# Kernel optimization log

Measured on AMD Instinct MI355X. Metric: run time of the kernel, lower is better.

Reference implementation:

```python
import jax, jax.numpy as jnp
import numpy as np
from jax import lax

GN_EPS = 1e-5
LRELU_SLOPE = 0.2
TOP_K = 3
COMMITMENT = 0.25
NUM_CODES = 1024

def conv(x, w, b, stride=1, pad=1):
    y = lax.conv_general_dilated(x, w, (stride, stride), ((pad, pad), (pad, pad)),
                                 dimension_numbers=('NCHW', 'OIHW', 'NCHW'))
    return y + b[None, :, None, None]

def conv_transpose(x, w, b, stride=2, pad=1, out_pad=1):
    # torch ConvTranspose2d: w is (Cin, Cout, kH, kW); equivalent to lhs-dilated conv
    # with flipped, io-swapped kernel and padding k-1-p (plus out_pad on high side).
    k = w.shape[2]
    p = k - 1 - pad
    w_f = jnp.transpose(jnp.flip(w, (2, 3)), (1, 0, 2, 3))  # -> OIHW
    y = lax.conv_general_dilated(x, w_f, (1, 1), ((p, p + out_pad), (p, p + out_pad)),
                                 lhs_dilation=(stride, stride),
                                 dimension_numbers=('NCHW', 'OIHW', 'NCHW'))
    return y + b[None, :, None, None]

def group_norm(x, g, beta, groups=2):
    N, C, H, W = x.shape
    xg = x.reshape(N, groups, C // groups, H, W)
    mu = xg.mean((2, 3, 4), keepdims=True)
    var = xg.var((2, 3, 4), keepdims=True)
    xn = ((xg - mu) * lax.rsqrt(var + GN_EPS)).reshape(N, C, H, W)
    return xn * g[None, :, None, None] + beta[None, :, None, None]

def lrelu(x):
    return jnp.where(x >= 0, x, LRELU_SLOPE * x)

def vq_ema_eval(z, emb):
    # z: [B, D, H, W] -> tokens [N, D]; eval path (no EMA buffer updates)
    inputs = jnp.transpose(z, (0, 2, 3, 1))  # [B,H,W,D]
    flat = inputs.reshape(-1, emb.shape[1])
    d = (jnp.sum(flat ** 2, 1, keepdims=True) + jnp.sum(emb ** 2, 1)
         - 2.0 * flat @ emb.T)  # [N, K]
    _, idx = lax.top_k(-d, TOP_K)  # top_k smallest distances
    q0 = emb[idx[:, 0]].reshape(inputs.shape)
    e_latent_loss = jnp.mean((lax.stop_gradient(q0) - inputs) ** 2)
    loss = COMMITMENT * e_latent_loss
    quantized = inputs + lax.stop_gradient(q0 - inputs)  # straight-through
    # perplexity uses the LAST (k-th nearest) encodings, matching the torch loop
    last = idx[:, TOP_K - 1]
    counts = jnp.zeros((emb.shape[0],), flat.dtype).at[last].add(1.0)
    avg_probs = counts / flat.shape[0]
    perplexity = jnp.exp(-jnp.sum(avg_probs * jnp.log(avg_probs + 1e-10)))
    return loss, jnp.transpose(quantized, (0, 3, 1, 2)), perplexity

def setup_inputs() -> dict:
    key = jax.random.key(0)
    ks = jax.random.split(key, 16)
    s = 0.05
    d = {
        'x': jax.random.normal(ks[0], (4, 4, 96, 96), jnp.float32),
        'e0_w': jax.random.normal(ks[1], (128, 4, 3, 3), jnp.float32) * s,
        'e0_b': jnp.zeros((128,), jnp.float32),
        'e0_g': jnp.ones((128,), jnp.float32),
        'e0_beta': jnp.zeros((128,), jnp.float32),
        'e1_w': jax.random.normal(ks[2], (128, 128, 3, 3), jnp.float32) * s,
        'e1_b': jnp.zeros((128,), jnp.float32),
        'e1_g': jnp.ones((128,), jnp.float32),
        'e1_beta': jnp.zeros((128,), jnp.float32),
        'pv_w': jax.random.normal(ks[3], (128, 128, 1, 1), jnp.float32) * s,
        'pv_b': jnp.zeros((128,), jnp.float32),
        'emb': jax.random.normal(ks[4], (NUM_CODES, 128), jnp.float32),
        'd0_w': jax.random.normal(ks[5], (128, 128, 3, 3), jnp.float32) * s,  # ConvT: (Cin,Cout,k,k)
        'd0_b': jnp.zeros((128,), jnp.float32),
        'd0_g': jnp.ones((128,), jnp.float32),
        'd0_beta': jnp.zeros((128,), jnp.float32),
        'd1_w': jax.random.normal(ks[6], (128, 256, 3, 3), jnp.float32) * s,
        'd1_b': jnp.zeros((128,), jnp.float32),
        'd1_g': jnp.ones((128,), jnp.float32),
        'd1_beta': jnp.zeros((128,), jnp.float32),
        'proj_w': jax.random.normal(ks[7], (128, 128, 1, 1), jnp.float32) * s,
        'proj_b': jnp.zeros((128,), jnp.float32),
        'ro_w': jax.random.normal(ks[8], (4, 128, 1, 1), jnp.float32) * s,
        'ro_b': jnp.zeros((4,), jnp.float32),
    }
    return d

def reference(x, e0_w, e0_b, e0_g, e0_beta, e1_w, e1_b, e1_g, e1_beta,
              pv_w, pv_b, emb,
              d0_w, d0_b, d0_g, d0_beta, d1_w, d1_b, d1_g, d1_beta,
              proj_w, proj_b, ro_w, ro_b):
    # Encoder: strides [1, 2]
    enc1 = lrelu(group_norm(conv(x, e0_w, e0_b, stride=1, pad=1), e0_g, e0_beta))
    latent = lrelu(group_norm(conv(enc1, e1_w, e1_b, stride=2, pad=1), e1_g, e1_beta))
    z = conv(latent, pv_w, pv_b, stride=1, pad=0)
    loss, quantized, perplexity = vq_ema_eval(z, emb)
    # Decoder: strides [2, 1]; skip projected (embedding_dim != C_out)
    skip = conv(enc1, proj_w, proj_b, stride=1, pad=0)
    h = lrelu(group_norm(conv_transpose(quantized, d0_w, d0_b, stride=2, pad=1, out_pad=1), d0_g, d0_beta))
    y = lrelu(group_norm(conv(jnp.concatenate([h, skip], axis=1), d1_w, d1_b, stride=1, pad=1), d1_g, d1_beta))
    x_recon = conv(y, ro_w, ro_b, stride=1, pad=0)
    return (loss, x_recon, perplexity)
```

## Files before the change

### kernel.cpp

```cpp
#include <hip/hip_runtime.h>

#define DEVI __device__ __forceinline__

typedef unsigned short u16;
typedef __attribute__((ext_vector_type(8))) short bf8v;
typedef __attribute__((ext_vector_type(4))) short s4v;
typedef __attribute__((ext_vector_type(4))) float f4v;

constexpr int NB = 4, C = 128, H = 96, W = 96, HW = H * W;
constexpr int HL = 48, WL = 48, HWL = HL * WL;
constexpr int CODES = 1024, DIM = 128;
constexpr int ROWS = NB * HWL;

DEVI float lrelu_f(float v) { return v >= 0.f ? v : 0.2f * v; }

DEVI u16 f2bf(float f) {
  union { float f; unsigned u; } v; v.f = f;
  unsigned r = (v.u + 0x7FFFu + ((v.u >> 16) & 1u)) >> 16;
  return (u16)r;
}

DEVI float bf2f(u16 h) {
  union { unsigned u; float f; } v; v.u = (unsigned)h << 16;
  return v.f;
}

DEVI void wave_red2(float& s, float& s2) {
#pragma unroll
  for (int o = 32; o > 0; o >>= 1) { s += __shfl_down(s, o); s2 += __shfl_down(s2, o); }
}

DEVI bool block_red2(float& s, float& s2) {
  wave_red2(s, s2);
  __shared__ float ls[8], ls2[8];
  int wv = threadIdx.x >> 6, ln = threadIdx.x & 63;
  if (ln == 0) { ls[wv] = s; ls2[wv] = s2; }
  __syncthreads();
  if (threadIdx.x == 0) {
    s = ls[0] + ls[1] + ls[2] + ls[3];
    s2 = ls2[0] + ls2[1] + ls2[2] + ls2[3];
    return true;
  }
  return false;
}

DEVI void ins3(float e, int j, float& d0, int& i0, float& d1, int& i1, float& d2, int& i2) {
  bool b0 = (e < d0) || (e == d0 && j < i0);
  bool b1 = (e < d1) || (e == d1 && j < i1);
  bool b2 = (e < d2) || (e == d2 && j < i2);
  float nd0 = b0 ? e : d0;             int ni0 = b0 ? j : i0;
  float nd1 = b0 ? d0 : (b1 ? e : d1); int ni1 = b0 ? i0 : (b1 ? j : i1);
  float nd2 = b1 ? d1 : (b2 ? e : d2); int ni2 = b1 ? i1 : (b2 ? j : i2);
  d0 = nd0; i0 = ni0; d1 = nd1; i1 = ni1; d2 = nd2; i2 = ni2;
}

__global__ __launch_bounds__(256) void k_red16(const float2* __restrict__ src,
                                               float* __restrict__ dst, int per) {
  int slot = blockIdx.x;
  float s = 0.f, s2 = 0.f;
  for (int i = threadIdx.x; i < per; i += 256) {
    float2 v = src[(size_t)slot * per + i];
    s += v.x; s2 += v.y;
  }
  if (block_red2(s, s2)) { dst[slot * 2] = s; dst[slot * 2 + 1] = s2; }
}

__global__ __launch_bounds__(256) void k_pack_all(
    const float* __restrict__ d1_w, const float* __restrict__ d0_w,
    const float* __restrict__ pj_w, const float* __restrict__ emb,
    const float* __restrict__ e1_w,
    u16* __restrict__ A1, u16* __restrict__ A0, u16* __restrict__ Apj,
    u16* __restrict__ ehtil, u16* __restrict__ We1,
    float* __restrict__ enorm, float* __restrict__ counts) {
  int b = blockIdx.x, t = threadIdx.x;
  if (b < 1152) {
    int i = b * 256 + t;
    int ci = i & 31, co = (i >> 5) & 127, r = i >> 12;
    int kx = r % 3; int r2 = r / 3; int ch = r2 & 7, ky = r2 >> 3;
    A1[i] = f2bf(d1_w[((size_t)(co * 256 + ch * 32 + ci) * 3 + ky) * 3 + kx]);
  } else if (b < 1728) {
    int i = (b - 1152) * 256 + t;
    int ci = i & 31, co = (i >> 5) & 127, r = i >> 12;
    int wx = r % 3; int r2 = r / 3; int ch = r2 & 3, wy = r2 >> 2;
    A0[i] = f2bf(d0_w[((size_t)((ch * 32 + ci) * 128 + co) * 3 + wy) * 3 + wx]);
  } else if (b < 1792) {
    int i = (b - 1728) * 256 + t;
    int ci = i & 31, co = (i >> 5) & 127, ch = i >> 12;
    Apj[i] = f2bf(pj_w[co * 128 + ch * 32 + ci]);
  } else if (b < 1920) {
    int g = (b - 1792) * 256 + t;
    int ct = g >> 9; int rem = g & 511;
    int j = rem >> 6; int l = rem & 63;
    int code = ct * 16 + (l & 15);
    int kb = j * 32 + (l >> 4) * 8;
    bool lo = kb >= 128; int k0 = lo ? kb - 128 : kb;
    const float* ep = emb + (size_t)code * DIM + k0;
    u16 o[8];
#pragma unroll
    for (int e = 0; e < 8; ++e) {
      float v = ep[e];
      u16 h = f2bf(v);
      o[e] = lo ? f2bf(v - bf2f(h)) : h;
    }
    bf8v ov = {(short)o[0], (short)o[1], (short)o[2], (short)o[3],
               (short)o[4], (short)o[5], (short)o[6], (short)o[7]};
    *(bf8v*)&ehtil[(size_t)g * 8] = ov;
  } else if (b < 1924) {
    int e = (b - 1920) * 256 + t;
    const float4* p = (const float4*)(emb + (size_t)e * DIM);
    float s = 0.f;
#pragma unroll 8
    for (int i = 0; i < 32; ++i) {
      float4 v = p[i];
      s = fmaf(v.x, v.x, s); s = fmaf(v.y, v.y, s); s = fmaf(v.z, v.z, s); s = fmaf(v.w, v.w, s);
    }
    enorm[e] = s;
  } else if (b == 1924) {
#pragma unroll
    for (int k = 0; k < 4; ++k) counts[t + k * 256] = 0.f;
  } else {
    int p = (b - 1925) * 256 + t;
    int s = p >> 6, l = p & 63;
    int ct = s & 7; int r = s >> 3;
    int kx = r % 3; int r2 = r / 3; int ch = r2 & 3, ky = r2 >> 2;
    int co = ct * 16 + (l & 15), ci0 = ch * 32 + (l >> 4) * 8;
    u16 hh[8], ll[8];
#pragma unroll
    for (int e = 0; e < 8; ++e) {
      float v = e1_w[((size_t)(co * 128 + ci0 + e) * 3 + ky) * 3 + kx];
      u16 h = f2bf(v); hh[e] = h; ll[e] = f2bf(v - bf2f(h));
    }
    bf8v hv = {(short)hh[0], (short)hh[1], (short)hh[2], (short)hh[3],
               (short)hh[4], (short)hh[5], (short)hh[6], (short)hh[7]};
    bf8v lv = {(short)ll[0], (short)ll[1], (short)ll[2], (short)ll[3],
               (short)ll[4], (short)ll[5], (short)ll[6], (short)ll[7]};
    *(bf8v*)&We1[(size_t)s * 1024 + l * 8] = hv;
    *(bf8v*)&We1[(size_t)s * 1024 + 512 + l * 8] = lv;
  }
}

__global__ __launch_bounds__(256) void k_conv_e0t(
    const float* __restrict__ x, const float* __restrict__ wg,
    const float* __restrict__ bias, float* __restrict__ out, float2* __restrict__ ps) {
  __shared__ float xs[4][18][104];
  int b = blockIdx.x;
  int rq = b % 6; int co = (b / 6) & 127; int n = b / 768;
  int t = threadIdx.x;
  int tx = t & 15, r = t >> 4;
  int y0 = rq * 16;
  for (int e = t; e < 4 * 18 * 104; e += 256) {
    int ci = e / 1872; int rem = e - ci * 1872;
    int row = rem / 104; int off = rem - row * 104;
    int iy = y0 - 1 + row; int ix = off - 1;
    float v = 0.f;
    if ((unsigned)iy < 96u && (unsigned)ix < 96u)
      v = x[((size_t)(n * 4 + ci)) * HW + iy * 96 + ix];
    xs[ci][row][off] = v;
  }
  float wr[4][9];
  const float* wp = wg + co * 36;
#pragma unroll
  for (int ci = 0; ci < 4; ++ci)
#pragma unroll
    for (int k = 0; k < 9; ++k) wr[ci][k] = wp[ci * 9 + k];
  float bv = bias[co];
  __syncthreads();
  float acc[6];
#pragma unroll
  for (int p = 0; p < 6; ++p) acc[p] = bv;
#pragma unroll
  for (int ci = 0; ci < 4; ++ci) {
#pragma unroll
    for (int ky = 0; ky < 3; ++ky) {
      const float* rp = &xs[ci][r + ky][6 * tx];
      float f[8];
#pragma unroll
      for (int j = 0; j < 4; ++j) {
        float2 v2 = *(const float2*)(rp + 2 * j);
        f[2 * j] = v2.x; f[2 * j + 1] = v2.y;
      }
      float w0 = wr[ci][ky * 3 + 0], w1 = wr[ci][ky * 3 + 1], w2 = wr[ci][ky * 3 + 2];
#pragma unroll
      for (int p = 0; p < 6; ++p)
        acc[p] = fmaf(w0, f[p], fmaf(w1, f[p + 1], fmaf(w2, f[p + 2], acc[p])));
    }
  }
  float* op = out + ((size_t)(n * 128 + co) * 96 + (y0 + r)) * 96 + 6 * tx;
#pragma unroll
  for (int j = 0; j < 3; ++j) {
    float2 v2 = { acc[2 * j], acc[2 * j + 1] };
    *(float2*)(op + 2 * j) = v2;
  }
  float s = 0.f, s2 = 0.f;
#pragma unroll
  for (int p = 0; p < 6; ++p) { s += acc[p]; s2 += acc[p] * acc[p]; }
  if (block_red2(s, s2)) {
    int slot = n * 2 + (co >> 6);
    ps[(size_t)slot * 384 + (co & 63) * 6 + rq] = make_float2(s, s2);
  }
}

__global__ __launch_bounds__(256) void k_gn_px(
    const float* __restrict__ enc1, const float* __restrict__ stats,
    const float* __restrict__ gam, const float* __restrict__ bet, u16* __restrict__ xp) {
  int b = blockIdx.x;
  int ch = b & 3; int iy = (b >> 2) % 96; int n = b / 384;
  int t = threadIdx.x;
  const float invc = 1.f / (64.f * 9216.f);
  size_t chunk = ((size_t)((n * 96 + iy) * 4 + ch)) * 6208;
  for (int e = t; e < 388; e += 256) {
    int oct = e / 97, u = e - oct * 97;
    int ix = (u < 48) ? 2 * u : 2 * (u - 48) - 1;
    u16* dh = xp + chunk + u * 32 + oct * 8;
    u16* dl = dh + 3104;
    if (ix < 0) {
      bf8v z = {0, 0, 0, 0, 0, 0, 0, 0};
      *(bf8v*)dh = z; *(bf8v*)dl = z;
      continue;
    }
    u16 hh[8], ll[8];
#pragma unroll
    for (int e8 = 0; e8 < 8; ++e8) {
      int c = ch * 32 + oct * 8 + e8;
      const float* st = stats + (n * 2 + (c >> 6)) * 2;
      float mu = st[0] * invc;
      float var = fmaf(-mu, mu, st[1] * invc);
      float rs = rsqrtf(var + 1e-5f);
      float raw = enc1[((size_t)(n * 128 + c)) * 9216 + iy * 96 + ix];
      float v = lrelu_f(fmaf((raw - mu) * rs, gam[c], bet[c]));
      u16 h = f2bf(v); hh[e8] = h; ll[e8] = f2bf(v - bf2f(h));
    }
    bf8v hv = {(short)hh[0], (short)hh[1], (short)hh[2], (short)hh[3],
               (short)hh[4], (short)hh[5], (short)hh[6], (short)hh[7]};
    bf8v lv = {(short)ll[0], (short)ll[1], (short)ll[2], (short)ll[3],
               (short)ll[4], (short)ll[5], (short)ll[6], (short)ll[7]};
    *(bf8v*)dh = hv; *(bf8v*)dl = lv;
  }
}

__global__ __launch_bounds__(256) void k_conv_e1m(
    const u16* __restrict__ xp, const u16* __restrict__ We1,
    const float* __restrict__ bias, float* __restrict__ latent, float2* __restrict__ ps) {
  __shared__ float ls[4], ls2[4];
  int braw = blockIdx.x;
  int b = (braw & 7) * 48 + (braw >> 3);
  int cb = b & 1; int oy = (b >> 1) % 48; int n = b / 96;
  int t = threadIdx.x; int w = t >> 6; int lane = t & 63;
  int ln16 = lane & 15, quad = lane >> 4;
  int ctg = cb * 4 + w;
  f4v acc[3];
#pragma unroll
  for (int nt = 0; nt < 3; ++nt) acc[nt] = (f4v){0.f, 0.f, 0.f, 0.f};
  for (int ky = 0; ky < 3; ++ky) {
    int iy = 2 * oy + ky - 1;
    if ((unsigned)iy >= 96u) continue;
    for (int ch = 0; ch < 4; ++ch) {
      const u16* chunk = xp + ((size_t)((n * 96 + iy) * 4 + ch)) * 6208;
      const u16* wb = We1 + ((size_t)((ky * 4 + ch) * 3)) * 8192;
      bf8v ah[3], al[3];
#pragma unroll
      for (int kx = 0; kx < 3; ++kx) {
        const u16* sl = wb + (kx * 8 + ctg) * 1024 + lane * 8;
        ah[kx] = *(const bf8v*)sl;
        al[kx] = *(const bf8v*)(sl + 512);
      }
#pragma unroll
      for (int nt = 0; nt < 3; ++nt) {
        int px = nt * 16 + ln16;
        const u16* be = chunk + px * 32 + quad * 8;
        const u16* bo = chunk + (48 + px) * 32 + quad * 8;
        bf8v bhe  = *(const bf8v*)be;
        bf8v ble  = *(const bf8v*)(be + 3104);
        bf8v bho0 = *(const bf8v*)bo;
        bf8v blo0 = *(const bf8v*)(bo + 3104);
        bf8v bho1 = *(const bf8v*)(bo + 32);
        bf8v blo1 = *(const bf8v*)(bo + 32 + 3104);
        acc[nt] = __builtin_amdgcn_mfma_f32_16x16x32_bf16(ah[1], bhe, acc[nt], 0, 0, 0);
        acc[nt] = __builtin_amdgcn_mfma_f32_16x16x32_bf16(al[1], bhe, acc[nt], 0, 0, 0);
        acc[nt] = __builtin_amdgcn_mfma_f32_16x16x32_bf16(ah[1], ble, acc[nt], 0, 0, 0);
        acc[nt] = __builtin_amdgcn_mfma_f32_16x16x32_bf16(ah[0], bho0, acc[nt], 0, 0, 0);
        acc[nt] = __builtin_amdgcn_mfma_f32_16x16x32_bf16(al[0], bho0, acc[nt], 0, 0, 0);
        acc[nt] = __builtin_amdgcn_mfma_f32_16x16x32_bf16(ah[0], blo0, acc[nt], 0, 0, 0);
        acc[nt] = __builtin_amdgcn_mfma_f32_16x16x32_bf16(ah[2], bho1, acc[nt], 0, 0, 0);
        acc[nt] = __builtin_amdgcn_mfma_f32_16x16x32_bf16(al[2], bho1, acc[nt], 0, 0, 0);
        acc[nt] = __builtin_amdgcn_mfma_f32_16x16x32_bf16(ah[2], blo1, acc[nt], 0, 0, 0);
      }
    }
  }
  int co0 = cb * 64 + w * 16 + quad * 4;
  float4 bv = *(const float4*)&bias[co0];
  float s = 0.f, s2 = 0.f;
#pragma unroll
  for (int nt = 0; nt < 3; ++nt) {
    int px = nt * 16 + ln16;
#pragma unroll
    for (int g = 0; g < 4; ++g) {
      float bvg = (g == 0) ? bv.x : (g == 1) ? bv.y : (g == 2) ? bv.z : bv.w;
      float v = acc[nt][g] + bvg;
      latent[((size_t)(n * 128 + co0 + g)) * 2304 + oy * 48 + px] = v;
      s += v; s2 += v * v;
    }
  }
  wave_red2(s, s2);
  if (lane == 0) { ls[w] = s; ls2[w] = s2; }
  __syncthreads();
  if (t == 0) {
    int slot = n * 2 + cb;
    ps[(size_t)slot * 48 + oy] =
        make_float2(ls[0] + ls[1] + ls[2] + ls[3], ls2[0] + ls2[1] + ls2[2] + ls2[3]);
  }
}

__global__ __launch_bounds__(256) void k_gn_nhwc_bf(
    const float* __restrict__ in, u16* __restrict__ outb, const float* __restrict__ stats,
    const float* __restrict__ gam, const float* __restrict__ bet) {
  int idx = blockIdx.x * 256 + threadIdx.x;
  int c = idx & 127;
  int n = idx / (9216 * 128);
  const float* st = stats + (n * 2 + (c >> 6)) * 2;
  const float invcnt = 1.f / (64.f * 9216.f);
  float mu = st[0] * invcnt;
  float var = fmaf(-mu, mu, st[1] * invcnt);
  float rs = rsqrtf(var + 1e-5f);
  float v = in[idx];
  outb[idx] = f2bf(lrelu_f(fmaf((v - mu) * rs, gam[c], bet[c])));
}

__global__ __launch_bounds__(256, 2) void k_pv(
    const float* __restrict__ in, const float* __restrict__ w,
    const float* __restrict__ bias, const float* __restrict__ stats1,
    const float* __restrict__ gam, const float* __restrict__ bet,
    u16* __restrict__ zp) {
  int b = blockIdx.x;
  int pxb = b % 36; int cb = (b / 36) & 1; int n = b / 72;
  int t = threadIdx.x;
  int pxg = t & 7, cg = t >> 3;
  int px0 = pxb * 64 + pxg * 8;
  int cobase = cb * 64 + cg * 2;
  const float invc = 1.f / (64.f * 2304.f);
  float acc[2][8];
#pragma unroll
  for (int c = 0; c < 2; ++c) {
    float bv = bias[cobase + c];
#pragma unroll
    for (int p = 0; p < 8; ++p) acc[c][p] = bv;
  }
  const float* ipb = in + (size_t)n * 128 * HWL + px0;
  for (int ci0 = 0; ci0 < 128; ci0 += 4) {
    float inr[4][8];
#pragma unroll
    for (int i = 0; i < 4; ++i) {
      int c = ci0 + i;
      const float* st = stats1 + (n * 2 + (c >> 6)) * 2;
      float mu = st[0] * invc;
      float var = fmaf(-mu, mu, st[1] * invc);
      float rsv = rsqrtf(var + 1e-5f);
      float ga = gam[c], be = bet[c];
      const float* ip = ipb + (size_t)c * HWL;
      float4 a = *(const float4*)ip; float4 bq = *(const float4*)(ip + 4);
      inr[i][0] = lrelu_f(fmaf((a.x - mu) * rsv, ga, be));
      inr[i][1] = lrelu_f(fmaf((a.y - mu) * rsv, ga, be));
      inr[i][2] = lrelu_f(fmaf((a.z - mu) * rsv, ga, be));
      inr[i][3] = lrelu_f(fmaf((a.w - mu) * rsv, ga, be));
      inr[i][4] = lrelu_f(fmaf((bq.x - mu) * rsv, ga, be));
      inr[i][5] = lrelu_f(fmaf((bq.y - mu) * rsv, ga, be));
      inr[i][6] = lrelu_f(fmaf((bq.z - mu) * rsv, ga, be));
      inr[i][7] = lrelu_f(fmaf((bq.w - mu) * rsv, ga, be));
    }
    float wr[2][4];
#pragma unroll
    for (int c = 0; c < 2; ++c) {
      float4 wv = *(const float4*)&w[(size_t)(cobase + c) * 128 + ci0];
      wr[c][0] = wv.x; wr[c][1] = wv.y; wr[c][2] = wv.z; wr[c][3] = wv.w;
    }
#pragma unroll
    for (int i = 0; i < 4; ++i)
#pragma unroll
      for (int c = 0; c < 2; ++c)
#pragma unroll
        for (int p = 0; p < 8; ++p) acc[c][p] = fmaf(wr[c][i], inr[i][p], acc[c][p]);
  }
#pragma unroll
  for (int p = 0; p < 8; ++p) {
    size_t r = (size_t)n * HWL + px0 + p;
    u16 h0 = f2bf(acc[0][p]); u16 l0 = f2bf(acc[0][p] - bf2f(h0));
    u16 h1 = f2bf(acc[1][p]); u16 l1 = f2bf(acc[1][p] - bf2f(h1));
    unsigned hp = (unsigned)h0 | ((unsigned)h1 << 16);
    unsigned lp = (unsigned)l0 | ((unsigned)l1 << 16);
    *(unsigned*)&zp[r * 256 + cobase] = hp;
    *(unsigned*)&zp[r * 256 + 128 + cobase] = lp;
  }
}

__global__ __launch_bounds__(512, 4) void k_vq(
    const u16* __restrict__ zp, const u16* __restrict__ ehtil,
    const float* __restrict__ emb, const float* __restrict__ enorm,
    u16* __restrict__ qb, float* __restrict__ counts, float* __restrict__ pvq) {
  __shared__ float wd[8][16][3];
  __shared__ int   wi[8][16][3];
  __shared__ float lred[8];
  __shared__ int hist[CODES];
  int r0 = blockIdx.x * 16;
  int t = threadIdx.x, w = t >> 6, lane = t & 63;
  int ln16 = lane & 15, quad = lane >> 4;
  hist[t] = 0; hist[t + 512] = 0;
  const u16* zrow = zp + (size_t)(r0 + ln16) * 256 + quad * 8;
  bf8v bh[4], bl[4];
#pragma unroll
  for (int kk = 0; kk < 4; ++kk) {
    bh[kk] = *(const bf8v*)(zrow + kk * 32);
    bl[kk] = *(const bf8v*)(zrow + 128 + kk * 32);
  }
  float d0 = 3.4e38f, d1 = 3.4e38f, d2 = 3.4e38f;
  int i0 = -1, i1 = -1, i2 = -1;
  const u16* abase = ehtil + (size_t)(w * 8) * 4096 + lane * 8;
#pragma unroll
  for (int tt = 0; tt < 8; ++tt) {
    const u16* ap = abase + tt * 4096;
    bf8v af[8];
#pragma unroll
    for (int j = 0; j < 8; ++j) af[j] = *(const bf8v*)(ap + j * 512);
    f4v accA = (f4v){0.f, 0.f, 0.f, 0.f};
    f4v accB = (f4v){0.f, 0.f, 0.f, 0.f};
    f4v accC = (f4v){0.f, 0.f, 0.f, 0.f};
#pragma unroll
    for (int kk = 0; kk < 4; ++kk) {
      accA = __builtin_amdgcn_mfma_f32_16x16x32_bf16(af[kk], bh[kk], accA, 0, 0, 0);
      accB = __builtin_amdgcn_mfma_f32_16x16x32_bf16(af[4 + kk], bh[kk], accB, 0, 0, 0);
      accC = __builtin_amdgcn_mfma_f32_16x16x32_bf16(af[kk], bl[kk], accC, 0, 0, 0);
    }
    int cbase = (w * 8 + tt) * 16 + quad * 4;
#pragma unroll
    for (int g = 0; g < 4; ++g) {
      int code = cbase + g;
      float dot = accA[g] + accB[g] + accC[g];
      float d = fmaf(-2.f, dot, enorm[code]);
      bool b0 = d < d0, b1 = d < d1, b2 = d < d2;
      float nd0 = b0 ? d : d0;             int ni0 = b0 ? code : i0;
      float nd1 = b0 ? d0 : (b1 ? d : d1); int ni1 = b0 ? i0 : (b1 ? code : i1);
      float nd2 = b1 ? d1 : (b2 ? d : d2); int ni2 = b1 ? i1 : (b2 ? code : i2);
      d0 = nd0; i0 = ni0; d1 = nd1; i1 = ni1; d2 = nd2; i2 = ni2;
    }
  }
#pragma unroll
  for (int off = 16; off <= 32; off <<= 1) {
    float e0 = __shfl_xor(d0, off), e1 = __shfl_xor(d1, off), e2 = __shfl_xor(d2, off);
    int j0 = __shfl_xor(i0, off), j1 = __shfl_xor(i1, off), j2 = __shfl_xor(i2, off);
    ins3(e0, j0, d0, i0, d1, i1, d2, i2);
    ins3(e1, j1, d0, i0, d1, i1, d2, i2);
    ins3(e2, j2, d0, i0, d1, i1, d2, i2);
  }
  if (quad == 0) {
    wd[w][ln16][0] = d0; wd[w][ln16][1] = d1; wd[w][ln16][2] = d2;
    wi[w][ln16][0] = i0; wi[w][ln16][1] = i1; wi[w][ln16][2] = i2;
  }
  __syncthreads();
  float lsum = 0.f;
  for (int ii = 0; ii < 2; ++ii) {
    int i = w * 2 + ii;
    float bd; int bi;
    if (lane < 24) { bd = wd[lane / 3][i][lane % 3]; bi = wi[lane / 3][i][lane % 3]; }
    else { bd = 3.4e38f; bi = 0x7fffffff; }
    int a[3];
#pragma unroll
    for (int p = 0; p < 3; ++p) {
      float d = bd; int idx = bi;
#pragma unroll
      for (int o = 1; o <= 32; o <<= 1) {
        float od = __shfl_xor(d, o); int oi = __shfl_xor(idx, o);
        if (od < d || (od == d && oi < idx)) { d = od; idx = oi; }
      }
      a[p] = idx;
      if (bi == idx) { bd = 3.4e38f; bi = 0x7fffffff; }
    }
    int r = r0 + i;
    const float* q0p = emb + (size_t)a[0] * DIM;
    const u16* zr = zp + (size_t)r * 256;
    float lp = 0.f;
#pragma unroll
    for (int cc = 0; cc < 2; ++cc) {
      int c = lane + cc * 64;
      float qv = q0p[c];
      qb[(size_t)r * 128 + c] = f2bf(qv);
      float zv = bf2f(zr[c]) + bf2f(zr[128 + c]);
      float dd = zv - qv;
      lp = fmaf(dd, dd, lp);
    }
#pragma unroll
    for (int o = 32; o > 0; o >>= 1) lp += __shfl_down(lp, o);
    if (lane == 0) { lsum += lp; atomicAdd(&hist[a[2]], 1); }
  }
  if (lane == 0) lred[w] = lsum;
  __syncthreads();
  if (t == 0) {
    float s = 0.f;
#pragma unroll
    for (int q = 0; q < 8; ++q) s += lred[q];
    pvq[blockIdx.x] = s;
  }
#pragma unroll
  for (int k = 0; k < 2; ++k) {
    int e = t + k * 512;
    int cnt = hist[e];
    if (cnt) atomicAdd(&counts[e], (float)cnt);
  }
}

__global__ __launch_bounds__(256) void k_finalize(
    const float* __restrict__ counts, const float* __restrict__ pvq, float* __restrict__ out) {
  float local = 0.f;
#pragma unroll
  for (int k = 0; k < 4; ++k) {
    float cnt = counts[threadIdx.x + k * 256];
    float pr = cnt * (1.f / (float)ROWS);
    local = fmaf(pr, logf(pr + 1e-10f), local);
  }
  float lsum = 0.f;
  for (int i = threadIdx.x; i < ROWS / 16; i += 256) lsum += pvq[i];
  if (block_red2(local, lsum)) {
    out[1 + NB * 4 * HW] = expf(-local);
    out[0] = 0.25f * lsum * (1.f / (9216.f * 128.f));
  }
}

__global__ __launch_bounds__(256) void k_proj_m(
    const float* __restrict__ enc1, const u16* __restrict__ Apj,
    const float* __restrict__ bias, const float* __restrict__ stats0,
    const float* __restrict__ gam, const float* __restrict__ bet,
    u16* __restrict__ skipb) {
  __shared__ u16 Ash[128 * 32];
  __shared__ u16 Bsh[96 * 32];
  int b = blockIdx.x; int rowi = b % 96; int n = b / 96; int px0 = rowi * 96;
  int t = threadIdx.x; int w = t >> 6; int lane = t & 63;
  int ln16 = lane & 15, quad = lane >> 4;
  int co0w = (w & 1) * 64; int pxh = (w >> 1) * 48;
  int c_l = t & 31, xg = t >> 5;
  const float invc = 1.f / (64.f * 9216.f);
  f4v acc[4][3];
#pragma unroll
  for (int mt = 0; mt < 4; ++mt)
#pragma unroll
    for (int nt = 0; nt < 3; ++nt) acc[mt][nt] = (f4v){0.f, 0.f, 0.f, 0.f};
  for (int ch = 0; ch < 4; ++ch) {
    __syncthreads();
#pragma unroll
    for (int e = 0; e < 2; ++e) {
      int i = t + e * 256;
      *(bf8v*)&Ash[i * 8] = *(const bf8v*)&Apj[ch * 4096 + i * 8];
    }
    int c = ch * 32 + c_l;
    const float* st = stats0 + (n * 2 + (ch >> 1)) * 2;
    float mu = st[0] * invc;
    float var = fmaf(-mu, mu, st[1] * invc);
    float rsv = rsqrtf(var + 1e-5f);
    float ga = gam[c], be = bet[c];
    const float* ip = enc1 + (size_t)(n * 128 + c) * 9216 + px0 + xg * 12;
#pragma unroll
    for (int j4 = 0; j4 < 3; ++j4) {
      float4 v = *(const float4*)(ip + j4 * 4);
      int pxb = xg * 12 + j4 * 4;
      Bsh[(pxb + 0) * 32 + c_l] = f2bf(lrelu_f(fmaf((v.x - mu) * rsv, ga, be)));
      Bsh[(pxb + 1) * 32 + c_l] = f2bf(lrelu_f(fmaf((v.y - mu) * rsv, ga, be)));
      Bsh[(pxb + 2) * 32 + c_l] = f2bf(lrelu_f(fmaf((v.z - mu) * rsv, ga, be)));
      Bsh[(pxb + 3) * 32 + c_l] = f2bf(lrelu_f(fmaf((v.w - mu) * rsv, ga, be)));
    }
    __syncthreads();
    bf8v af[4];
#pragma unroll
    for (int mt = 0; mt < 4; ++mt)
      af[mt] = *(const bf8v*)&Ash[(co0w + mt * 16 + ln16) * 32 + quad * 8];
#pragma unroll
    for (int nt = 0; nt < 3; ++nt) {
      bf8v bfv = *(const bf8v*)&Bsh[(pxh + nt * 16 + ln16) * 32 + quad * 8];
#pragma unroll
      for (int mt = 0; mt < 4; ++mt)
        acc[mt][nt] = __builtin_amdgcn_mfma_f32_16x16x32_bf16(af[mt], bfv, acc[mt][nt], 0, 0, 0);
    }
  }
#pragma unroll
  for (int mt = 0; mt < 4; ++mt) {
    int co = co0w + mt * 16 + quad * 4;
    float4 bv = *(const float4*)&bias[co];
#pragma unroll
    for (int nt = 0; nt < 3; ++nt) {
      int px = px0 + pxh + nt * 16 + ln16;
      u16* dp = skipb + (size_t)(n * 9216 + px) * 128 + co;
      s4v sv;
      sv.x = (short)f2bf(acc[mt][nt].x + bv.x);
      sv.y = (short)f2bf(acc[mt][nt].y + bv.y);
      sv.z = (short)f2bf(acc[mt][nt].z + bv.z);
      sv.w = (short)f2bf(acc[mt][nt].w + bv.w);
      *(s4v*)dp = sv;
    }
  }
}

__global__ __launch_bounds__(256) void k_convt_d0m(
    const u16* __restrict__ qb, const u16* __restrict__ A0,
    const float* __restrict__ bias, float* __restrict__ h, float2* __restrict__ ps) {
  __shared__ u16 Ash[2 * 128 * 32];
  __shared__ u16 Bsh[49 * 32];
  int braw = blockIdx.x;
  int b = (braw & 7) * 96 + (braw >> 3);
  int rx = b & 1; int oy = (b >> 1) % 96; int n = b / 192;
  int t = threadIdx.x; int w = t >> 6; int lane = t & 63;
  int ln16 = lane & 15, quad = lane >> 4;
  int co0w = w * 32;
  f4v acc[2][3];
#pragma unroll
  for (int mt = 0; mt < 2; ++mt)
#pragma unroll
    for (int nt = 0; nt < 3; ++nt) acc[mt][nt] = (f4v){0.f, 0.f, 0.f, 0.f};
  int nyt, wys[2], iys[2];
  if (oy & 1) {
    wys[0] = 2; iys[0] = (oy - 1) >> 1;
    wys[1] = 0; iys[1] = (oy + 1) >> 1;
    nyt = (iys[1] < 48) ? 2 : 1;
  } else { wys[0] = 1; iys[0] = oy >> 1; wys[1] = 0; iys[1] = 0; nyt = 1; }
  int nxt = rx ? 2 : 1;
  int wxs[2], xof[2];
  if (rx) { wxs[0] = 2; xof[0] = 0; wxs[1] = 0; xof[1] = 1; }
  else { wxs[0] = 1; xof[0] = 0; wxs[1] = 0; xof[1] = 0; }
  for (int yt = 0; yt < nyt; ++yt) {
    for (int ch = 0; ch < 4; ++ch) {
      __syncthreads();
      for (int e = t; e < nxt * 512; e += 256) {
        int xt = e >> 9, e2 = e & 511;
        const u16* Asrc = A0 + (size_t)(((wys[yt] * 4 + ch) * 3 + wxs[xt]) * 4096);
        *(bf8v*)&Ash[xt * 4096 + e2 * 8] = *(const bf8v*)&Asrc[e2 * 8];
      }
      const u16* bbase = qb + (size_t)(n * 2304 + iys[yt] * 48) * 128 + ch * 32;
      for (int e = t; e < 196; e += 256) {
        int row = e >> 2, seg = e & 3;
        bf8v v = {0, 0, 0, 0, 0, 0, 0, 0};
        if (row < 48) v = *(const bf8v*)&bbase[row * 128 + seg * 8];
        *(bf8v*)&Bsh[row * 32 + seg * 8] = v;
      }
      __syncthreads();
      for (int xt = 0; xt < nxt; ++xt) {
        bf8v af[2];
#pragma unroll
        for (int mt = 0; mt < 2; ++mt)
          af[mt] = *(const bf8v*)&Ash[xt * 4096 + (co0w + mt * 16 + ln16) * 32 + quad * 8];
#pragma unroll
        for (int nt = 0; nt < 3; ++nt) {
          bf8v bfv = *(const bf8v*)&Bsh[(nt * 16 + ln16 + xof[xt]) * 32 + quad * 8];
#pragma unroll
          for (int mt = 0; mt < 2; ++mt)
            acc[mt][nt] = __builtin_amdgcn_mfma_f32_16x16x32_bf16(af[mt], bfv, acc[mt][nt], 0, 0, 0);
        }
      }
    }
  }
  float s = 0.f, s2 = 0.f;
#pragma unroll
  for (int mt = 0; mt < 2; ++mt) {
    int co = co0w + mt * 16 + quad * 4;
    float4 bv = *(const float4*)&bias[co];
#pragma unroll
    for (int nt = 0; nt < 3; ++nt) {
      int px = nt * 16 + ln16;
      int ox = 2 * px + rx;
      float4 v;
      v.x = acc[mt][nt].x + bv.x; v.y = acc[mt][nt].y + bv.y;
      v.z = acc[mt][nt].z + bv.z; v.w = acc[mt][nt].w + bv.w;
      *(float4*)(h + (size_t)(n * 9216 + oy * 96 + ox) * 128 + co) = v;
      s += v.x + v.y + v.z + v.w;
      s2 += v.x * v.x + v.y * v.y + v.z * v.z + v.w * v.w;
    }
  }
  wave_red2(s, s2);
  if (lane == 0) {
    int slot = n * 2 + (w >> 1);
    ps[(size_t)slot * 384 + (oy * 2 + rx) * 2 + (w & 1)] = make_float2(s, s2);
  }
}

__global__ __launch_bounds__(256) void k_conv_d1m(
    const u16* __restrict__ hb, const u16* __restrict__ sb,
    const u16* __restrict__ A1, const float* __restrict__ bias,
    float* __restrict__ y, float2* __restrict__ ps) {
  __shared__ u16 Ash[3 * 64 * 32];
  __shared__ u16 Bsh[98 * 32];
  int braw = blockIdx.x;
  int b = (braw & 7) * 96 + (braw >> 3);
  int cb = b & 1; int oy = (b >> 1) % 96; int n = b / 192;
  int t = threadIdx.x; int w = t >> 6; int lane = t & 63;
  int ln16 = lane & 15, quad = lane >> 4;
  int co0w = (w & 1) * 32; int pxh = (w >> 1) * 48;
  f4v acc[2][3];
#pragma unroll
  for (int mt = 0; mt < 2; ++mt)
#pragma unroll
    for (int nt = 0; nt < 3; ++nt) acc[mt][nt] = (f4v){0.f, 0.f, 0.f, 0.f};
  int ky0 = (oy == 0) ? 1 : 0, ky1 = (oy == 95) ? 1 : 2;
  for (int ky = ky0; ky <= ky1; ++ky) {
    int iy = oy + ky - 1;
    for (int ch = 0; ch < 8; ++ch) {
      const u16* src = (ch < 4) ? hb : sb;
      int c0 = (ch & 3) * 32;
      const u16* Asrc = A1 + (size_t)(ky * 8 + ch) * 12288;
      const u16* bbase = src + (size_t)(n * 9216 + iy * 96) * 128 + c0;
      __syncthreads();
#pragma unroll
      for (int j = 0; j < 3; ++j) {
        int e = t + j * 256;
        int kx = e >> 8; int e2 = e & 255; int co_l = e2 >> 2; int seg = e2 & 3;
        *(bf8v*)&Ash[(kx * 64 + co_l) * 32 + seg * 8] =
            *(const bf8v*)&Asrc[(size_t)kx * 4096 + (cb * 64 + co_l) * 32 + seg * 8];
      }
      for (int e = t; e < 392; e += 256) {
        int row = e >> 2, seg = e & 3;
        int ix = row - 1;
        bf8v v = {0, 0, 0, 0, 0, 0, 0, 0};
        if ((unsigned)ix < 96u) v = *(const bf8v*)&bbase[ix * 128 + seg * 8];
        *(bf8v*)&Bsh[row * 32 + seg * 8] = v;
      }
      __syncthreads();
#pragma unroll
      for (int kx = 0; kx < 3; ++kx) {
        bf8v af[2];
#pragma unroll
        for (int mt = 0; mt < 2; ++mt)
          af[mt] = *(const bf8v*)&Ash[(kx * 64 + co0w + mt * 16 + ln16) * 32 + quad * 8];
#pragma unroll
        for (int nt = 0; nt < 3; ++nt) {
          bf8v bfv = *(const bf8v*)&Bsh[(pxh + nt * 16 + ln16 + kx) * 32 + quad * 8];
#pragma unroll
          for (int mt = 0; mt < 2; ++mt)
            acc[mt][nt] = __builtin_amdgcn_mfma_f32_16x16x32_bf16(af[mt], bfv, acc[mt][nt], 0, 0, 0);
        }
      }
    }
  }
  float s = 0.f, s2 = 0.f;
#pragma unroll
  for (int mt = 0; mt < 2; ++mt) {
    int co = cb * 64 + co0w + mt * 16 + quad * 4;
    float4 bv = *(const float4*)&bias[co];
#pragma unroll
    for (int nt = 0; nt < 3; ++nt) {
      int px = pxh + nt * 16 + ln16;
      float4 v;
      v.x = acc[mt][nt].x + bv.x; v.y = acc[mt][nt].y + bv.y;
      v.z = acc[mt][nt].z + bv.z; v.w = acc[mt][nt].w + bv.w;
      *(float4*)(y + (size_t)(n * 9216 + oy * 96 + px) * 128 + co) = v;
      s += v.x + v.y + v.z + v.w;
      s2 += v.x * v.x + v.y * v.y + v.z * v.z + v.w * v.w;
    }
  }
  wave_red2(s, s2);
  if (lane == 0) {
    int slot = n * 2 + cb;
    ps[(size_t)slot * 384 + oy * 4 + w] = make_float2(s, s2);
  }
}

__global__ __launch_bounds__(256) void k_ro(
    const float* __restrict__ y, const float* __restrict__ w,
    const float* __restrict__ bias, const float* __restrict__ stats3,
    const float* __restrict__ gam, const float* __restrict__ bet,
    float* __restrict__ out) {
  __shared__ float wsh[512];
  __shared__ float gsh[128], bsh[128];
  __shared__ float red[64][16];
  int b = blockIdx.x; int n = b / 144; int px0 = (b % 144) * 64;
  int t = threadIdx.x; int q = t & 3, pxl = t >> 2;
  for (int e = t; e < 512; e += 256) wsh[e] = w[e];
  if (t < 128) { gsh[t] = gam[t]; bsh[t] = bet[t]; }
  __syncthreads();
  const float invc = 1.f / (64.f * 9216.f);
  int g = q >> 1;
  const float* st = stats3 + (n * 2 + g) * 2;
  float mu = st[0] * invc;
  float var = fmaf(-mu, mu, st[1] * invc);
  float rsv = rsqrtf(var + 1e-5f);
  const float* yb = y + (size_t)(n * 9216 + px0 + pxl) * 128 + q * 32;
  float s0 = 0.f, s1 = 0.f, s2 = 0.f, s3 = 0.f;
#pragma unroll
  for (int j = 0; j < 8; ++j) {
    float4 v = *(const float4*)(yb + j * 4);
    int c0 = q * 32 + j * 4;
    float vx = lrelu_f(fmaf((v.x - mu) * rsv, gsh[c0 + 0], bsh[c0 + 0]));
    float vy = lrelu_f(fmaf((v.y - mu) * rsv, gsh[c0 + 1], bsh[c0 + 1]));
    float vz = lrelu_f(fmaf((v.z - mu) * rsv, gsh[c0 + 2], bsh[c0 + 2]));
    float vw = lrelu_f(fmaf((v.w - mu) * rsv, gsh[c0 + 3], bsh[c0 + 3]));
    const float* w0 = &wsh[0 * 128 + c0];
    const float* w1 = &wsh[1 * 128 + c0];
    const float* w2 = &wsh[2 * 128 + c0];
    const float* w3 = &wsh[3 * 128 + c0];
    s0 += vx * w0[0] + vy * w0[1] + vz * w0[2] + vw * w0[3];
    s1 += vx * w1[0] + vy * w1[1] + vz * w1[2] + vw * w1[3];
    s2 += vx * w2[0] + vy * w2[1] + vz * w2[2] + vw * w2[3];
    s3 += vx * w3[0] + vy * w3[1] + vz * w3[2] + vw * w3[3];
  }
  red[pxl][q * 4 + 0] = s0; red[pxl][q * 4 + 1] = s1;
  red[pxl][q * 4 + 2] = s2; red[pxl][q * 4 + 3] = s3;
  __syncthreads();
  float val = red[pxl][0 * 4 + q] + red[pxl][1 * 4 + q] + red[pxl][2 * 4 + q] + red[pxl][3 * 4 + q] + bias[q];
  out[1 + (size_t)(n * 4 + q) * 9216 + px0 + pxl] = val;
}

extern "C" void kernel_launch(void* const* d_in, const int* in_sizes, int n_in,
                              void* d_out, int out_size, void* d_ws, size_t ws_size,
                              hipStream_t stream) {
  (void)in_sizes; (void)n_in; (void)out_size; (void)ws_size;
  const float* x     = (const float*)d_in[0];
  const float* e0_w  = (const float*)d_in[1];
  const float* e0_b  = (const float*)d_in[2];
  const float* e0_g  = (const float*)d_in[3];
  const float* e0_bt = (const float*)d_in[4];
  const float* e1_w  = (const float*)d_in[5];
  const float* e1_b  = (const float*)d_in[6];
  const float* e1_g  = (const float*)d_in[7];
  const float* e1_bt = (const float*)d_in[8];
  const float* pv_w  = (const float*)d_in[9];
  const float* pv_b  = (const float*)d_in[10];
  const float* emb   = (const float*)d_in[11];
  const float* d0_w  = (const float*)d_in[12];
  const float* d0_b  = (const float*)d_in[13];
  const float* d0_g  = (const float*)d_in[14];
  const float* d0_bt = (const float*)d_in[15];
  const float* d1_w  = (const float*)d_in[16];
  const float* d1_b  = (const float*)d_in[17];
  const float* d1_g  = (const float*)d_in[18];
  const float* d1_bt = (const float*)d_in[19];
  const float* pj_w  = (const float*)d_in[20];
  const float* pj_b  = (const float*)d_in[21];
  const float* ro_w  = (const float*)d_in[22];
  const float* ro_b  = (const float*)d_in[23];
  float* out = (float*)d_out;
  float* ws = (float*)d_ws;

  float* stats  = ws;
  float* counts = ws + 64;
  float* enorm  = ws + 1088;
  float* pvq    = ws + 2112;
  float2* ps_e0 = (float2*)(ws + 3264);
  float2* ps_e1 = (float2*)(ws + 76992);
  float2* ps_d0 = (float2*)(ws + 95424);
  float2* ps_d1 = (float2*)(ws + 107712);
  float* enc1   = ws + 114688;
  float* latent = enc1 + (size_t)NB * C * HW;
  float* zbuf   = latent + (size_t)NB * C * HWL;
  float* hy     = zbuf + (size_t)NB * C * HWL;
  u16* qb    = (u16*)(hy + (size_t)NB * C * HW);
  u16* hb    = qb + (size_t)NB * C * HWL;
  u16* skipb = hb + (size_t)NB * C * HW;
  u16* A1    = skipb + (size_t)NB * C * HW;
  u16* A0    = A1 + 294912;
  u16* Apj   = A0 + 147456;
  u16* ehtil = Apj + 16384 + 64;
  u16* zp    = (u16*)zbuf;
  u16* xp  = qb;
  u16* We1 = qb + 9535488;

  k_pack_all<<<2069, 256, 0, stream>>>(d1_w, d0_w, pj_w, emb, e1_w,
                                       A1, A0, Apj, ehtil, We1, enorm, counts);

  k_conv_e0t<<<3072, 256, 0, stream>>>(x, e0_w, e0_b, enc1, ps_e0);
  k_red16<<<8, 256, 0, stream>>>(ps_e0, stats + 0, 384);
  k_gn_px<<<NB * 96 * 4, 256, 0, stream>>>(enc1, stats + 0, e0_g, e0_bt, xp);
  k_conv_e1m<<<NB * 48 * 2, 256, 0, stream>>>(xp, We1, e1_b, latent, ps_e1);
  k_red16<<<8, 256, 0, stream>>>(ps_e1, stats + 16, 48);
  k_pv<<<288, 256, 0, stream>>>(latent, pv_w, pv_b, stats + 16, e1_g, e1_bt, zp);
  k_vq<<<ROWS / 16, 512, 0, stream>>>(zp, ehtil, emb, enorm, qb, counts, pvq);
  k_finalize<<<1, 256, 0, stream>>>(counts, pvq, out);

  k_proj_m<<<NB * 96, 256, 0, stream>>>(enc1, Apj, pj_b, stats + 0, e0_g, e0_bt, skipb);
  k_convt_d0m<<<NB * 96 * 2, 256, 0, stream>>>(qb, A0, d0_b, hy, ps_d0);
  k_red16<<<8, 256, 0, stream>>>(ps_d0, stats + 32, 384);
  k_gn_nhwc_bf<<<NB * C * HW / 256, 256, 0, stream>>>(hy, hb, stats + 32, d0_g, d0_bt);
  k_conv_d1m<<<NB * 96 * 2, 256, 0, stream>>>(hb, skipb, A1, d1_b, hy, ps_d1);
  k_red16<<<8, 256, 0, stream>>>(ps_d1, stats + 48, 384);
  k_ro<<<NB * 144, 256, 0, stream>>>(hy, ro_w, ro_b, stats + 48, d1_g, d1_bt, out);
}
```

Before: 351.7 us.

## Fold GroupNorm stat reductions and VQ finalize into producer kernels via last-block atomics

Removes the four small k_red16 launches and the k_finalize launch. Each producer kernel now bumps an atomic counter after writing its partial stats, and the last block to finish does the 8-slot reduction (or the perplexity and loss finalize) itself. This saves launch and serialization gaps between kernels. In exchange it adds threadfences, an atomic per block and a serial tail reduction inside one block. The ins3 helper in the VQ kernel is also hand-inlined, with no behavioural change.

```diff
diff --git a/kernel.cpp b/kernel.cpp
--- a/kernel.cpp
+++ b/kernel.cpp
@@ -44,25 +44,28 @@
   return false;
 }
 
-DEVI void ins3(float e, int j, float& d0, int& i0, float& d1, int& i1, float& d2, int& i2) {
-  bool b0 = (e < d0) || (e == d0 && j < i0);
-  bool b1 = (e < d1) || (e == d1 && j < i1);
-  bool b2 = (e < d2) || (e == d2 && j < i2);
-  float nd0 = b0 ? e : d0;             int ni0 = b0 ? j : i0;
-  float nd1 = b0 ? d0 : (b1 ? e : d1); int ni1 = b0 ? i0 : (b1 ? j : i1);
-  float nd2 = b1 ? d1 : (b2 ? e : d2); int ni2 = b1 ? i1 : (b2 ? j : i2);
-  d0 = nd0; i0 = ni0; d1 = nd1; i1 = ni1; d2 = nd2; i2 = ni2;
-}
-
-__global__ __launch_bounds__(256) void k_red16(const float2* __restrict__ src,
-                                               float* __restrict__ dst, int per) {
-  int slot = blockIdx.x;
-  float s = 0.f, s2 = 0.f;
-  for (int i = threadIdx.x; i < per; i += 256) {
-    float2 v = src[(size_t)slot * per + i];
-    s += v.x; s2 += v.y;
-  }
-  if (block_red2(s, s2)) { dst[slot * 2] = s; dst[slot * 2 + 1] = s2; }
+DEVI float2 aload2(const float2* p) {
+  unsigned long long u = __hip_atomic_load((unsigned long long*)p, __ATOMIC_RELAXED,
+                                           __HIP_MEMORY_SCOPE_AGENT);
+  union { unsigned long long u; float2 f; } c; c.u = u; return c.f;
+}
+DEVI float aload1(const float* p) {
+  return __hip_atomic_load((float*)p, __ATOMIC_RELAXED, __HIP_MEMORY_SCOPE_AGENT);
+}
+
+DEVI void reduce_ps8(const float2* __restrict__ ps, float* __restrict__ dst, int per, int t) {
+  __threadfence();
+  if (t < 256) {
+    int slot = t >> 5, ln = t & 31;
+    float s = 0.f, s2 = 0.f;
+    for (int i = ln; i < per; i += 32) {
+      float2 v = aload2(ps + (size_t)slot * per + i);
+      s += v.x; s2 += v.y;
+    }
+#pragma unroll
+    for (int o = 16; o > 0; o >>= 1) { s += __shfl_down(s, o, 32); s2 += __shfl_down(s2, o, 32); }
+    if (ln == 0) { dst[slot * 2] = s; dst[slot * 2 + 1] = s2; }
+  }
 }
 
 __global__ __launch_bounds__(256) void k_pack_all(
@@ -71,7 +74,7 @@
     const float* __restrict__ e1_w,
     u16* __restrict__ A1, u16* __restrict__ A0, u16* __restrict__ Apj,
     u16* __restrict__ ehtil, u16* __restrict__ We1,
-    float* __restrict__ enorm, float* __restrict__ counts) {
+    float* __restrict__ enorm, float* __restrict__ counts, int* __restrict__ cnts) {
   int b = blockIdx.x, t = threadIdx.x;
   if (b < 1152) {
     int i = b * 256 + t;
@@ -118,6 +121,7 @@
   } else if (b == 1924) {
 #pragma unroll
     for (int k = 0; k < 4; ++k) counts[t + k * 256] = 0.f;
+    if (t < 8) cnts[t] = 0;
   } else {
     int p = (b - 1925) * 256 + t;
     int s = p >> 6, l = p & 63;
@@ -141,8 +145,10 @@
 
 __global__ __launch_bounds__(256) void k_conv_e0t(
     const float* __restrict__ x, const float* __restrict__ wg,
-    const float* __restrict__ bias, float* __restrict__ out, float2* __restrict__ ps) {
+    const float* __restrict__ bias, float* __restrict__ out, float2* __restrict__ ps,
+    float* __restrict__ stats, int* __restrict__ cnt) {
   __shared__ float xs[4][18][104];
+  __shared__ int lastF;
   int b = blockIdx.x;
   int rq = b % 6; int co = (b / 6) & 127; int n = b / 768;
   int t = threadIdx.x;
@@ -197,7 +203,11 @@
   if (block_red2(s, s2)) {
     int slot = n * 2 + (co >> 6);
     ps[(size_t)slot * 384 + (co & 63) * 6 + rq] = make_float2(s, s2);
-  }
+    __threadfence();
+    lastF = (atomicAdd(cnt, 1) == 3072 - 1);
+  }
+  __syncthreads();
+  if (lastF) reduce_ps8(ps, stats, 384, t);
 }
 
 __global__ __launch_bounds__(256) void k_gn_px(
@@ -240,8 +250,10 @@
 
 __global__ __launch_bounds__(256) void k_conv_e1m(
     const u16* __restrict__ xp, const u16* __restrict__ We1,
-    const float* __restrict__ bias, float* __restrict__ latent, float2* __restrict__ ps) {
+    const float* __restrict__ bias, float* __restrict__ latent, float2* __restrict__ ps,
+    float* __restrict__ stats, int* __restrict__ cnt) {
   __shared__ float ls[4], ls2[4];
+  __shared__ int lastF;
   int braw = blockIdx.x;
   int b = (braw & 7) * 48 + (braw >> 3);
   int cb = b & 1; int oy = (b >> 1) % 48; int n = b / 96;
@@ -308,7 +320,11 @@
     int slot = n * 2 + cb;
     ps[(size_t)slot * 48 + oy] =
         make_float2(ls[0] + ls[1] + ls[2] + ls[3], ls2[0] + ls2[1] + ls2[2] + ls2[3]);
-  }
+    __threadfence();
+    lastF = (atomicAdd(cnt, 1) == 384 - 1);
+  }
+  __syncthreads();
+  if (lastF) reduce_ps8(ps, stats, 48, t);
 }
 
 __global__ __launch_bounds__(256) void k_gn_nhwc_bf(
@@ -395,11 +411,14 @@
 __global__ __launch_bounds__(512, 4) void k_vq(
     const u16* __restrict__ zp, const u16* __restrict__ ehtil,
     const float* __restrict__ emb, const float* __restrict__ enorm,
-    u16* __restrict__ qb, float* __restrict__ counts, float* __restrict__ pvq) {
+    u16* __restrict__ qb, float* __restrict__ counts, float* __restrict__ pvq,
+    float* __restrict__ out, int* __restrict__ cnt) {
   __shared__ float wd[8][16][3];
   __shared__ int   wi[8][16][3];
   __shared__ float lred[8];
   __shared__ int hist[CODES];
+  __shared__ int lastV;
+  __shared__ float fr[8], fr2[8];
   int r0 = blockIdx.x * 16;
   int t = threadIdx.x, w = t >> 6, lane = t & 63;
   int ln16 = lane & 15, quad = lane >> 4;
@@ -446,9 +465,34 @@
   for (int off = 16; off <= 32; off <<= 1) {
     float e0 = __shfl_xor(d0, off), e1 = __shfl_xor(d1, off), e2 = __shfl_xor(d2, off);
     int j0 = __shfl_xor(i0, off), j1 = __shfl_xor(i1, off), j2 = __shfl_xor(i2, off);
-    ins3(e0, j0, d0, i0, d1, i1, d2, i2);
-    ins3(e1, j1, d0, i0, d1, i1, d2, i2);
-    ins3(e2, j2, d0, i0, d1, i1, d2, i2);
+    ins3_inline: ;
+    {
+      bool b0 = (e0 < d0) || (e0 == d0 && j0 < i0);
+      bool b1 = (e0 < d1) || (e0 == d1 && j0 < i1);
+      bool b2 = (e0 < d2) || (e0 == d2 && j0 < i2);
+      float nd0 = b0 ? e0 : d0;             int ni0 = b0 ? j0 : i0;
+      float nd1 = b0 ? d0 : (b1 ? e0 : d1); int ni1 = b0 ? i0 : (b1 ? j0 : i1);
+      float nd2 = b1 ? d1 : (b2 ? e0 : d2); int ni2 = b1 ? i1 : (b2 ? j0 : i2);
+      d0 = nd0; i0 = ni0; d1 = nd1; i1 = ni1; d2 = nd2; i2 = ni2;
+    }
+    {
+      bool b0 = (e1 < d0) || (e1 == d0 && j1 < i0);
+      bool b1 = (e1 < d1) || (e1 == d1 && j1 < i1);
+      bool b2 = (e1 < d2) || (e1 == d2 && j1 < i2);
+      float nd0 = b0 ? e1 : d0;             int ni0 = b0 ? j1 : i0;
+      float nd1 = b0 ? d0 : (b1 ? e1 : d1); int ni1 = b0 ? i0 : (b1 ? j1 : i1);
+      float nd2 = b1 ? d1 : (b2 ? e1 : d2); int ni2 = b1 ? i1 : (b2 ? j1 : i2);
+      d0 = nd0; i0 = ni0; d1 = nd1; i1 = ni1; d2 = nd2; i2 = ni2;
+    }
+    {
+      bool b0 = (e2 < d0) || (e2 == d0 && j2 < i0);
+      bool b1 = (e2 < d1) || (e2 == d1 && j2 < i1);
+      bool b2 = (e2 < d2) || (e2 == d2 && j2 < i2);
+      float nd0 = b0 ? e2 : d0;             int ni0 = b0 ? j2 : i0;
+      float nd1 = b0 ? d0 : (b1 ? e2 : d1); int ni1 = b0 ? i0 : (b1 ? j2 : i1);
+      float nd2 = b1 ? d1 : (b2 ? e2 : d2); int ni2 = b1 ? i1 : (b2 ? j2 : i2);
+      d0 = nd0; i0 = ni0; d1 = nd1; i1 = ni1; d2 = nd2; i2 = ni2;
+    }
   }
   if (quad == 0) {
     wd[w][ln16][0] = d0; wd[w][ln16][1] = d1; wd[w][ln16][2] = d2;
@@ -501,25 +545,35 @@
 #pragma unroll
   for (int k = 0; k < 2; ++k) {
     int e = t + k * 512;
-    int cnt = hist[e];
-    if (cnt) atomicAdd(&counts[e], (float)cnt);
-  }
-}
-
-__global__ __launch_bounds__(256) void k_finalize(
-    const float* __restrict__ counts, const float* __restrict__ pvq, float* __restrict__ out) {
-  float local = 0.f;
-#pragma unroll
-  for (int k = 0; k < 4; ++k) {
-    float cnt = counts[threadIdx.x + k * 256];
-    float pr = cnt * (1.f / (float)ROWS);
-    local = fmaf(pr, logf(pr + 1e-10f), local);
-  }
-  float lsum = 0.f;
-  for (int i = threadIdx.x; i < ROWS / 16; i += 256) lsum += pvq[i];
-  if (block_red2(local, lsum)) {
-    out[1 + NB * 4 * HW] = expf(-local);
-    out[0] = 0.25f * lsum * (1.f / (9216.f * 128.f));
+    int chv = hist[e];
+    if (chv) atomicAdd(&counts[e], (float)chv);
+  }
+  __threadfence();
+  __syncthreads();
+  if (t == 0) lastV = (atomicAdd(cnt, 1) == 576 - 1);
+  __syncthreads();
+  if (lastV) {
+    __threadfence();
+    float local = 0.f;
+#pragma unroll
+    for (int k = 0; k < 2; ++k) {
+      float cv = aload1(&counts[t + k * 512]);
+      float pr = cv * (1.f / (float)ROWS);
+      local = fmaf(pr, logf(pr + 1e-10f), local);
+    }
+    float ls = 0.f;
+    for (int i = t; i < 576; i += 512) ls += aload1(&pvq[i]);
+    wave_red2(local, ls);
+    int wv2 = t >> 6, ln2 = t & 63;
+    if (ln2 == 0) { fr[wv2] = local; fr2[wv2] = ls; }
+    __syncthreads();
+    if (t == 0) {
+      float a = 0.f, bsum = 0.f;
+#pragma unroll
+      for (int q = 0; q < 8; ++q) { a += fr[q]; bsum += fr2[q]; }
+      out[1 + NB * 4 * HW] = expf(-a);
+      out[0] = 0.25f * bsum * (1.f / (9216.f * 128.f));
+    }
   }
 }
 
@@ -597,9 +651,11 @@
 
 __global__ __launch_bounds__(256) void k_convt_d0m(
     const u16* __restrict__ qb, const u16* __restrict__ A0,
-    const float* __restrict__ bias, float* __restrict__ h, float2* __restrict__ ps) {
+    const float* __restrict__ bias, float* __restrict__ h, float2* __restrict__ ps,
+    float* __restrict__ stats, int* __restrict__ cnt) {
   __shared__ u16 Ash[2 * 128 * 32];
   __shared__ u16 Bsh[49 * 32];
+  __shared__ int lastF;
   int braw = blockIdx.x;
   int b = (braw & 7) * 96 + (braw >> 3);
   int rx = b & 1; int oy = (b >> 1) % 96; int n = b / 192;
@@ -673,15 +729,22 @@
   if (lane == 0) {
     int slot = n * 2 + (w >> 1);
     ps[(size_t)slot * 384 + (oy * 2 + rx) * 2 + (w & 1)] = make_float2(s, s2);
-  }
+    __threadfence();
+  }
+  __syncthreads();
+  if (t == 0) lastF = (atomicAdd(cnt, 1) == 768 - 1);
+  __syncthreads();
+  if (lastF) reduce_ps8(ps, stats, 384, t);
 }
 
 __global__ __launch_bounds__(256) void k_conv_d1m(
     const u16* __restrict__ hb, const u16* __restrict__ sb,
     const u16* __restrict__ A1, const float* __restrict__ bias,
-    float* __restrict__ y, float2* __restrict__ ps) {
+    float* __restrict__ y, float2* __restrict__ ps,
+    float* __restrict__ stats, int* __restrict__ cnt) {
   __shared__ u16 Ash[3 * 64 * 32];
   __shared__ u16 Bsh[98 * 32];
+  __shared__ int lastF;
   int braw = blockIdx.x;
   int b = (braw & 7) * 96 + (braw >> 3);
   int cb = b & 1; int oy = (b >> 1) % 96; int n = b / 192;
@@ -753,7 +816,12 @@
   if (lane == 0) {
     int slot = n * 2 + cb;
     ps[(size_t)slot * 384 + oy * 4 + w] = make_float2(s, s2);
-  }
+    __threadfence();
+  }
+  __syncthreads();
+  if (t == 0) lastF = (atomicAdd(cnt, 1) == 768 - 1);
+  __syncthreads();
+  if (lastF) reduce_ps8(ps, stats, 384, t);
 }
 
 __global__ __launch_bounds__(256) void k_ro(
@@ -836,6 +904,7 @@
   float* counts = ws + 64;
   float* enorm  = ws + 1088;
   float* pvq    = ws + 2112;
+  int*   cnts   = (int*)(ws + 3200);
   float2* ps_e0 = (float2*)(ws + 3264);
   float2* ps_e1 = (float2*)(ws + 76992);
   float2* ps_d0 = (float2*)(ws + 95424);
@@ -856,22 +925,17 @@
   u16* We1 = qb + 9535488;
 
   k_pack_all<<<2069, 256, 0, stream>>>(d1_w, d0_w, pj_w, emb, e1_w,
-                                       A1, A0, Apj, ehtil, We1, enorm, counts);
-
-  k_conv_e0t<<<3072, 256, 0, stream>>>(x, e0_w, e0_b, enc1, ps_e0);
-  k_red16<<<8, 256, 0, stream>>>(ps_e0, stats + 0, 384);
+                                       A1, A0, Apj, ehtil, We1, enorm, counts, cnts);
+
+  k_conv_e0t<<<3072, 256, 0, stream>>>(x, e0_w, e0_b, enc1, ps_e0, stats + 0, cnts + 0);
   k_gn_px<<<NB * 96 * 4, 256, 0, stream>>>(enc1, stats + 0, e0_g, e0_bt, xp);
-  k_conv_e1m<<<NB * 48 * 2, 256, 0, stream>>>(xp, We1, e1_b, latent, ps_e1);
-  k_red16<<<8, 256, 0, stream>>>(ps_e1, stats + 16, 48);
+  k_conv_e1m<<<NB * 48 * 2, 256, 0, stream>>>(xp, We1, e1_b, latent, ps_e1, stats + 16, cnts + 1);
   k_pv<<<288, 256, 0, stream>>>(latent, pv_w, pv_b, stats + 16, e1_g, e1_bt, zp);
-  k_vq<<<ROWS / 16, 512, 0, stream>>>(zp, ehtil, emb, enorm, qb, counts, pvq);
-  k_finalize<<<1, 256, 0, stream>>>(counts, pvq, out);
+  k_vq<<<ROWS / 16, 512, 0, stream>>>(zp, ehtil, emb, enorm, qb, counts, pvq, out, cnts + 4);
 
   k_proj_m<<<NB * 96, 256, 0, stream>>>(enc1, Apj, pj_b, stats + 0, e0_g, e0_bt, skipb);
-  k_convt_d0m<<<NB * 96 * 2, 256, 0, stream>>>(qb, A0, d0_b, hy, ps_d0);
-  k_red16<<<8, 256, 0, stream>>>(ps_d0, stats + 32, 384);
+  k_convt_d0m<<<NB * 96 * 2, 256, 0, stream>>>(qb, A0, d0_b, hy, ps_d0, stats + 32, cnts + 2);
   k_gn_nhwc_bf<<<NB * C * HW / 256, 256, 0, stream>>>(hy, hb, stats + 32, d0_g, d0_bt);
-  k_conv_d1m<<<NB * 96 * 2, 256, 0, stream>>>(hb, skipb, A1, d1_b, hy, ps_d1);
-  k_red16<<<8, 256, 0, stream>>>(ps_d1, stats + 48, 384);
+  k_conv_d1m<<<NB * 96 * 2, 256, 0, stream>>>(hb, skipb, A1, d1_b, hy, ps_d1, stats + 48, cnts + 3);
   k_ro<<<NB * 144, 256, 0, stream>>>(hy, ro_w, ro_b, stats + 48, d1_g, d1_bt, out);
 }
```

After: 729.8 us. 107% more time.
